# Optimization experiments

Hardware: AMD Instinct MI355X
Metric: run time of the kernel (lower is better)

Reference implementation:

```python
import jax, jax.numpy as jnp
import numpy as np

N_ATOMS = 100000
N_BONDS = 200000
N_MOLS = 4000
ATOMS_PER_MOL = 25
MAX_NB = 6
ATOM_FDIM = 133
BOND_FDIM = 14
HIDDEN = 300
DEPTH = 3


def setup_inputs() -> dict:
    key = jax.random.key(0)
    ks = jax.random.split(key, 8)
    f_atoms = jax.random.normal(ks[0], (N_ATOMS, ATOM_FDIM), dtype=jnp.float32)
    f_bonds = jax.random.normal(ks[1], (N_BONDS, BOND_FDIM), dtype=jnp.float32)
    # incoming-bond lists per atom (irregular gather targets)
    a2b = jax.random.randint(ks[2], (N_ATOMS, MAX_NB), 0, N_BONDS, dtype=jnp.int32)
    # source atom of each directed bond
    b2a = jax.random.randint(ks[3], (N_BONDS,), 0, N_ATOMS, dtype=jnp.int32)
    # reverse bond: directed bonds come in pairs (2i, 2i+1)
    b2revb = (jnp.arange(N_BONDS, dtype=jnp.int32) ^ 1)
    # contiguous [start, size] per molecule
    starts = jnp.arange(N_MOLS, dtype=jnp.int32) * ATOMS_PER_MOL
    sizes = jnp.full((N_MOLS,), ATOMS_PER_MOL, dtype=jnp.int32)
    a_scope = jnp.stack([starts, sizes], axis=1)
    W_i = jax.random.normal(ks[4], (HIDDEN, ATOM_FDIM + BOND_FDIM), dtype=jnp.float32) * 0.05
    W_h = jax.random.normal(ks[5], (HIDDEN, HIDDEN), dtype=jnp.float32) * 0.05
    W_o = jax.random.normal(ks[6], (HIDDEN, ATOM_FDIM + HIDDEN), dtype=jnp.float32) * 0.05
    b_o = jax.random.normal(ks[7], (HIDDEN,), dtype=jnp.float32) * 0.05
    return {"f_atoms": f_atoms, "f_bonds": f_bonds, "a2b": a2b, "b2a": b2a,
            "b2revb": b2revb, "a_scope": a_scope, "W_i": W_i, "W_h": W_h,
            "W_o": W_o, "b_o": b_o}


def reference(f_atoms, f_bonds, a2b, b2a, b2revb, a_scope, W_i, W_h, W_o, b_o):
    # initial directed-bond messages: [f_atoms[src], f_bonds] -> Linear -> ReLU
    input_feats = jnp.concatenate([f_atoms[b2a], f_bonds], axis=1)  # (E, 147)
    message = jax.nn.relu(input_feats @ W_i.T)  # (E, H)
    for _ in range(DEPTH - 1):
        nei_a_message = message[a2b].sum(axis=1)          # (V, H) gather+sum
        nei_message = nei_a_message[b2a] - message[b2revb]  # (E, H)
        message = jax.nn.relu(nei_message @ W_h.T)
    a_message = message[a2b].sum(axis=1)  # (V, H)
    atom_hiddens = jax.nn.relu(jnp.concatenate([f_atoms, a_message], axis=1) @ W_o.T + b_o)
    # vectorized scope mean-pool (scopes are contiguous ranges)
    starts = a_scope[:, 0]
    sizes = a_scope[:, 1]
    seg_ids = jnp.searchsorted(starts, jnp.arange(atom_hiddens.shape[0]), side='right') - 1
    sums = jax.ops.segment_sum(atom_hiddens, seg_ids, num_segments=N_MOLS)
    denom = jnp.maximum(sizes, 1).astype(atom_hiddens.dtype)[:, None]
    mol_vecs = jnp.where((sizes > 0)[:, None], sums / denom, 0.0)
    return mol_vecs
```

## Files before the change

kernel.cpp:

```cpp
#include <hip/hip_runtime.h>
#include <hip/hip_bf16.h>
#include <stdint.h>

#define N_ATOMS   100000
#define N_BONDS   200000
#define N_MOLS    4000
#define MAX_NB    6
#define ATOM_FDIM 133
#define BOND_FDIM 14
#define HIDDEN    300
#define NPAD      320
#define KPAD_I    160
#define KPAD_H    320
#define KPAD_O    448

typedef __attribute__((ext_vector_type(8))) short          bf16x8;
typedef __attribute__((ext_vector_type(8))) unsigned short u16x8;
typedef __attribute__((ext_vector_type(4))) float          f32x4;

__device__ __forceinline__ float bf2f(unsigned short u) {
  union { unsigned int i; float f; } v; v.i = ((unsigned int)u) << 16; return v.f;
}
__device__ __forceinline__ unsigned short f2bf(float f) {
  union { float f; unsigned int i; } v; v.f = f;
  unsigned int u = v.i;
  return (unsigned short)((u + 0x7fffu + ((u >> 16) & 1u)) >> 16);
}

__global__ void convw_kernel(const float* __restrict__ w, unsigned short* __restrict__ o,
                             int N, int K, int KP) {
  int total = NPAD * KP;
  for (int idx = blockIdx.x * 256 + threadIdx.x; idx < total; idx += gridDim.x * 256) {
    int n = idx / KP, k = idx - n * KP;
    float v = (n < N && k < K) ? w[n * K + k] : 0.f;
    o[idx] = f2bf(v);
  }
}

__global__ void agg_kernel(const unsigned short* __restrict__ msg,
                           const int* __restrict__ a2b,
                           unsigned short* __restrict__ nei) {
  int idx = blockIdx.x * 256 + threadIdx.x;
  const int total = N_ATOMS * (NPAD / 8);
  if (idx >= total) return;
  int a  = idx / (NPAD / 8);
  int kc = (idx - a * (NPAD / 8)) * 8;
  float s[8];
#pragma unroll
  for (int e = 0; e < 8; e++) s[e] = 0.f;
#pragma unroll
  for (int j = 0; j < MAX_NB; j++) {
    int b = a2b[a * MAX_NB + j];
    u16x8 v = *(const u16x8*)&msg[(size_t)b * NPAD + kc];
#pragma unroll
    for (int e = 0; e < 8; e++) s[e] += bf2f(v[e]);
  }
  u16x8 o;
#pragma unroll
  for (int e = 0; e < 8; e++) o[e] = f2bf(s[e]);
  *(u16x8*)&nei[(size_t)a * NPAD + kc] = o;
}

template<int SRC>
__global__ __launch_bounds__(256) void gemm64_kernel(
    const float* __restrict__ f_atoms, const float* __restrict__ f_bonds,
    const int* __restrict__ b2a, const int* __restrict__ b2revb,
    const unsigned short* __restrict__ nei,
    const unsigned short* msgin,
    const unsigned short* __restrict__ W,
    const float* __restrict__ bias,
    unsigned short* out, int M, int KP) {
  __shared__ __align__(16) unsigned short As[64 * 32];

  const int b0   = blockIdx.x * 64;
  const int tid  = threadIdx.x;
  const int lane = tid & 63;
  const int wave = tid >> 6;
  const int sr   = tid >> 2;
  const int skc  = (tid & 3) * 8;

  int row = b0 + sr;
  if (row >= M) row = M - 1;
  int gatherRow = 0, revRow = 0;
  if (SRC == 0 || SRC == 1) gatherRow = b2a[row];
  if (SRC == 1) revRow = b2revb[row];

  f32x4 acc[4][5];
#pragma unroll
  for (int m = 0; m < 4; m++)
#pragma unroll
    for (int n = 0; n < 5; n++) acc[m][n] = (f32x4){0.f, 0.f, 0.f, 0.f};

  const int nbase = wave * 80;
  const unsigned short* Wl = W + (size_t)(nbase + (lane & 15)) * KP + ((lane >> 4) * 8);
  const int a_off = (lane & 15) * 32 + (lane >> 4) * 8;

  const int nsteps = KP / 32;
  for (int ks = 0; ks < nsteps; ks++) {
    const int k0 = ks * 32;
    unsigned short vals[8];
    if (SRC == 0) {
#pragma unroll
      for (int j = 0; j < 8; j++) {
        int k = k0 + skc + j;
        float v = 0.f;
        if (k < ATOM_FDIM)                  v = f_atoms[(size_t)gatherRow * ATOM_FDIM + k];
        else if (k < ATOM_FDIM + BOND_FDIM) v = f_bonds[(size_t)row * BOND_FDIM + (k - ATOM_FDIM)];
        vals[j] = f2bf(v);
      }
    } else if (SRC == 1) {
      u16x8 n8 = *(const u16x8*)&nei[(size_t)gatherRow * NPAD + k0 + skc];
      u16x8 m8 = *(const u16x8*)&msgin[(size_t)revRow * NPAD + k0 + skc];
#pragma unroll
      for (int j = 0; j < 8; j++) vals[j] = f2bf(bf2f(n8[j]) - bf2f(m8[j]));
    } else {
#pragma unroll
      for (int j = 0; j < 8; j++) {
        int k = k0 + skc + j;
        float v = 0.f;
        if (k < ATOM_FDIM)               v = f_atoms[(size_t)row * ATOM_FDIM + k];
        else if (k < ATOM_FDIM + HIDDEN) v = bf2f(nei[(size_t)row * NPAD + (k - ATOM_FDIM)]);
        vals[j] = f2bf(v);
      }
    }
    __syncthreads();
    *(u16x8*)&As[sr * 32 + skc] = *(const u16x8*)vals;
    __syncthreads();

    bf16x8 afrag[4];
#pragma unroll
    for (int m = 0; m < 4; m++) afrag[m] = *(const bf16x8*)&As[a_off + m * 16 * 32];
#pragma unroll
    for (int nf = 0; nf < 5; nf++) {
      bf16x8 bfrag = *(const bf16x8*)(Wl + (size_t)nf * 16 * KP + k0);
#pragma unroll
      for (int m = 0; m < 4; m++)
        acc[m][nf] = __builtin_amdgcn_mfma_f32_16x16x32_bf16(afrag[m], bfrag, acc[m][nf], 0, 0, 0);
    }
  }

#pragma unroll
  for (int m = 0; m < 4; m++) {
#pragma unroll
    for (int r = 0; r < 4; r++) {
      int orow = b0 + m * 16 + (lane >> 4) * 4 + r;
      if (orow >= M) continue;
#pragma unroll
      for (int nf = 0; nf < 5; nf++) {
        int ocol = nbase + nf * 16 + (lane & 15);
        float v = acc[m][nf][r];
        if (SRC == 2) v += (ocol < HIDDEN) ? bias[ocol] : 0.f;
        v = v > 0.f ? v : 0.f;
        out[(size_t)orow * NPAD + ocol] = f2bf(v);
      }
    }
  }
}

__global__ void readout_kernel(const unsigned short* __restrict__ hidden,
                               const int* __restrict__ a_scope,
                               float* __restrict__ out) {
  int idx = blockIdx.x * 256 + threadIdx.x;
  const int total = N_MOLS * HIDDEN;
  if (idx >= total) return;
  int m = idx / HIDDEN, c = idx - m * HIDDEN;
  int start = a_scope[m * 2], size = a_scope[m * 2 + 1];
  float s = 0.f;
  for (int i = 0; i < size; i++) s += bf2f(hidden[(size_t)(start + i) * NPAD + c]);
  out[idx] = (size > 0) ? s / (float)size : 0.f;
}

extern "C" void kernel_launch(void* const* d_in, const int* in_sizes, int n_in,
                              void* d_out, int out_size, void* d_ws, size_t ws_size,
                              hipStream_t stream) {
  const float* f_atoms = (const float*)d_in[0];
  const float* f_bonds = (const float*)d_in[1];
  const int*   a2b     = (const int*)d_in[2];
  const int*   b2a     = (const int*)d_in[3];
  const int*   b2revb  = (const int*)d_in[4];
  const int*   a_scope = (const int*)d_in[5];
  const float* W_i     = (const float*)d_in[6];
  const float* W_h     = (const float*)d_in[7];
  const float* W_o     = (const float*)d_in[8];
  const float* b_o     = (const float*)d_in[9];
  float* out = (float*)d_out;

  char* ws = (char*)d_ws;
  size_t off = 0;
  auto alloc = [&](size_t bytes) { size_t o = off; off += (bytes + 255) & ~(size_t)255; return o; };
  unsigned short* msg    = (unsigned short*)(ws + alloc((size_t)N_BONDS * NPAD * 2));
  unsigned short* nei    = (unsigned short*)(ws + alloc((size_t)N_ATOMS * NPAD * 2));
  unsigned short* hidden = (unsigned short*)(ws + alloc((size_t)N_ATOMS * NPAD * 2));
  unsigned short* Wi_bf  = (unsigned short*)(ws + alloc((size_t)NPAD * KPAD_I * 2));
  unsigned short* Wh_bf  = (unsigned short*)(ws + alloc((size_t)NPAD * KPAD_H * 2));
  unsigned short* Wo_bf  = (unsigned short*)(ws + alloc((size_t)NPAD * KPAD_O * 2));

  convw_kernel<<<(NPAD * KPAD_I + 255) / 256, 256, 0, stream>>>(W_i, Wi_bf, HIDDEN, ATOM_FDIM + BOND_FDIM, KPAD_I);
  convw_kernel<<<(NPAD * KPAD_H + 255) / 256, 256, 0, stream>>>(W_h, Wh_bf, HIDDEN, HIDDEN, KPAD_H);
  convw_kernel<<<(NPAD * KPAD_O + 255) / 256, 256, 0, stream>>>(W_o, Wo_bf, HIDDEN, ATOM_FDIM + HIDDEN, KPAD_O);

  const int gb = N_BONDS / 64;
  const int ga = (N_ATOMS + 63) / 64;

  gemm64_kernel<0><<<gb, 256, 0, stream>>>(f_atoms, f_bonds, b2a, b2revb, nullptr, nullptr,
                                           Wi_bf, nullptr, msg, N_BONDS, KPAD_I);
  for (int d = 0; d < 2; d++) {
    agg_kernel<<<(N_ATOMS * (NPAD / 8)) / 256, 256, 0, stream>>>(msg, a2b, nei);
    gemm64_kernel<1><<<gb, 256, 0, stream>>>(f_atoms, f_bonds, b2a, b2revb, nei, msg,
                                             Wh_bf, nullptr, msg, N_BONDS, KPAD_H);
  }
  agg_kernel<<<(N_ATOMS * (NPAD / 8)) / 256, 256, 0, stream>>>(msg, a2b, nei);
  gemm64_kernel<2><<<ga, 256, 0, stream>>>(f_atoms, f_bonds, b2a, b2revb, nei, nullptr,
                                           Wo_bf, b_o, hidden, N_ATOMS, KPAD_O);
  readout_kernel<<<(N_MOLS * HIDDEN + 255) / 256, 256, 0, stream>>>(hidden, a_scope, out);
}
```

Baseline: 732.1 us.

## Stage full A tile in LDS up front with batched gathers, drop per-step barriers

Each GEMM block now gathers its whole K extent of the A operand into shared memory before the MFMA loop. Loads are issued in groups of five 16-byte chunks so many irregular gathers are in flight at once, and the tile is stored in fragment order. This removes the two __syncthreads per K-step and the serialized gather-then-compute pattern. K padding becomes a compile-time constant and launch bounds request two blocks per CU. The cost is much larger LDS use (up to about 57KB for the output GEMM), which may cap occupancy.

```diff
diff --git a/kernel.cpp b/kernel.cpp
--- a/kernel.cpp
+++ b/kernel.cpp
@@ -62,22 +62,56 @@
 }
 
 template<int SRC>
-__global__ __launch_bounds__(256) void gemm64_kernel(
+__device__ __forceinline__ u16x8 stage_load(
+    int ks, int q, int row, int gatherRow, int revRow,
+    const float* __restrict__ f_atoms, const float* __restrict__ f_bonds,
+    const unsigned short* __restrict__ nei, const unsigned short* msgin) {
+  const int kc = ks * 32 + q * 8;
+  u16x8 r;
+  if (SRC == 1) {
+    u16x8 n8 = *(const u16x8*)&nei[(size_t)gatherRow * NPAD + kc];
+    u16x8 m8 = *(const u16x8*)&msgin[(size_t)revRow * NPAD + kc];
+#pragma unroll
+    for (int j = 0; j < 8; j++) r[j] = f2bf(bf2f(n8[j]) - bf2f(m8[j]));
+  } else if (SRC == 0) {
+#pragma unroll
+    for (int j = 0; j < 8; j++) {
+      int k = kc + j; float v = 0.f;
+      if (k < ATOM_FDIM)                  v = f_atoms[(size_t)gatherRow * ATOM_FDIM + k];
+      else if (k < ATOM_FDIM + BOND_FDIM) v = f_bonds[(size_t)row * BOND_FDIM + (k - ATOM_FDIM)];
+      r[j] = f2bf(v);
+    }
+  } else {
+#pragma unroll
+    for (int j = 0; j < 8; j++) {
+      int k = kc + j; float v = 0.f;
+      if (k < ATOM_FDIM)               v = f_atoms[(size_t)row * ATOM_FDIM + k];
+      else if (k < ATOM_FDIM + HIDDEN) v = bf2f(nei[(size_t)row * NPAD + (k - ATOM_FDIM)]);
+      r[j] = f2bf(v);
+    }
+  }
+  return r;
+}
+
+template<int SRC>
+__global__ __launch_bounds__(256, 2) void gemm64_kernel(
     const float* __restrict__ f_atoms, const float* __restrict__ f_bonds,
     const int* __restrict__ b2a, const int* __restrict__ b2revb,
     const unsigned short* __restrict__ nei,
     const unsigned short* msgin,
     const unsigned short* __restrict__ W,
     const float* __restrict__ bias,
-    unsigned short* out, int M, int KP) {
-  __shared__ __align__(16) unsigned short As[64 * 32];
+    unsigned short* out, int M) {
+  constexpr int KP  = (SRC == 0) ? KPAD_I : (SRC == 1) ? KPAD_H : KPAD_O;
+  constexpr int NST = KP / 32;
+  __shared__ __align__(16) unsigned short As[NST * 2048];
 
   const int b0   = blockIdx.x * 64;
   const int tid  = threadIdx.x;
   const int lane = tid & 63;
   const int wave = tid >> 6;
   const int sr   = tid >> 2;
-  const int skc  = (tid & 3) * 8;
+  const int q    = tid & 3;
 
   int row = b0 + sr;
   if (row >= M) row = M - 1;
@@ -85,6 +119,26 @@
   if (SRC == 0 || SRC == 1) gatherRow = b2a[row];
   if (SRC == 1) revRow = b2revb[row];
 
+  const int dbase = (sr >> 4) * 512 + (q * 16 + (sr & 15)) * 8;
+
+  constexpr int G = 5;
+#pragma unroll
+  for (int ks0 = 0; ks0 < NST; ks0 += G) {
+    u16x8 vals[G];
+#pragma unroll
+    for (int j = 0; j < G; j++) {
+      const int ks = ks0 + j;
+      if (ks < NST)
+        vals[j] = stage_load<SRC>(ks, q, row, gatherRow, revRow, f_atoms, f_bonds, nei, msgin);
+    }
+#pragma unroll
+    for (int j = 0; j < G; j++) {
+      const int ks = ks0 + j;
+      if (ks < NST) *(u16x8*)&As[ks * 2048 + dbase] = vals[j];
+    }
+  }
+  __syncthreads();
+
   f32x4 acc[4][5];
 #pragma unroll
   for (int m = 0; m < 4; m++)
@@ -93,46 +147,16 @@
 
   const int nbase = wave * 80;
   const unsigned short* Wl = W + (size_t)(nbase + (lane & 15)) * KP + ((lane >> 4) * 8);
-  const int a_off = (lane & 15) * 32 + (lane >> 4) * 8;
-
-  const int nsteps = KP / 32;
-  for (int ks = 0; ks < nsteps; ks++) {
-    const int k0 = ks * 32;
-    unsigned short vals[8];
-    if (SRC == 0) {
-#pragma unroll
-      for (int j = 0; j < 8; j++) {
-        int k = k0 + skc + j;
-        float v = 0.f;
-        if (k < ATOM_FDIM)                  v = f_atoms[(size_t)gatherRow * ATOM_FDIM + k];
-        else if (k < ATOM_FDIM + BOND_FDIM) v = f_bonds[(size_t)row * BOND_FDIM + (k - ATOM_FDIM)];
-        vals[j] = f2bf(v);
-      }
-    } else if (SRC == 1) {
-      u16x8 n8 = *(const u16x8*)&nei[(size_t)gatherRow * NPAD + k0 + skc];
-      u16x8 m8 = *(const u16x8*)&msgin[(size_t)revRow * NPAD + k0 + skc];
-#pragma unroll
-      for (int j = 0; j < 8; j++) vals[j] = f2bf(bf2f(n8[j]) - bf2f(m8[j]));
-    } else {
-#pragma unroll
-      for (int j = 0; j < 8; j++) {
-        int k = k0 + skc + j;
-        float v = 0.f;
-        if (k < ATOM_FDIM)               v = f_atoms[(size_t)row * ATOM_FDIM + k];
-        else if (k < ATOM_FDIM + HIDDEN) v = bf2f(nei[(size_t)row * NPAD + (k - ATOM_FDIM)]);
-        vals[j] = f2bf(v);
-      }
-    }
-    __syncthreads();
-    *(u16x8*)&As[sr * 32 + skc] = *(const u16x8*)vals;
-    __syncthreads();
-
+
+#pragma unroll
+  for (int ks = 0; ks < NST; ks++) {
     bf16x8 afrag[4];
 #pragma unroll
-    for (int m = 0; m < 4; m++) afrag[m] = *(const bf16x8*)&As[a_off + m * 16 * 32];
+    for (int m = 0; m < 4; m++)
+      afrag[m] = *(const bf16x8*)&As[ks * 2048 + m * 512 + lane * 8];
 #pragma unroll
     for (int nf = 0; nf < 5; nf++) {
-      bf16x8 bfrag = *(const bf16x8*)(Wl + (size_t)nf * 16 * KP + k0);
+      bf16x8 bfrag = *(const bf16x8*)(Wl + (size_t)nf * 16 * KP + ks * 32);
 #pragma unroll
       for (int m = 0; m < 4; m++)
         acc[m][nf] = __builtin_amdgcn_mfma_f32_16x16x32_bf16(afrag[m], bfrag, acc[m][nf], 0, 0, 0);
@@ -203,14 +227,14 @@
   const int ga = (N_ATOMS + 63) / 64;
 
   gemm64_kernel<0><<<gb, 256, 0, stream>>>(f_atoms, f_bonds, b2a, b2revb, nullptr, nullptr,
-                                           Wi_bf, nullptr, msg, N_BONDS, KPAD_I);
+                                           Wi_bf, nullptr, msg, N_BONDS);
   for (int d = 0; d < 2; d++) {
     agg_kernel<<<(N_ATOMS * (NPAD / 8)) / 256, 256, 0, stream>>>(msg, a2b, nei);
     gemm64_kernel<1><<<gb, 256, 0, stream>>>(f_atoms, f_bonds, b2a, b2revb, nei, msg,
-                                             Wh_bf, nullptr, msg, N_BONDS, KPAD_H);
+                                             Wh_bf, nullptr, msg, N_BONDS);
   }
   agg_kernel<<<(N_ATOMS * (NPAD / 8)) / 256, 256, 0, stream>>>(msg, a2b, nei);
   gemm64_kernel<2><<<ga, 256, 0, stream>>>(f_atoms, f_bonds, b2a, b2revb, nei, nullptr,
-                                           Wo_bf, b_o, hidden, N_ATOMS, KPAD_O);
+                                           Wo_bf, b_o, hidden, N_ATOMS);
   readout_kernel<<<(N_MOLS * HIDDEN + 255) / 256, 256, 0, stream>>>(hidden, a_scope, out);
 }
```

After: 730.4 us. About the same (-0.2%).
